# Kernel optimization log

Hardware: AMD Instinct MI355X
Metric: run time of the kernel (lower is better)

The kernel has to match this reference:

```python
import jax, jax.numpy as jnp
import numpy as np

B, L, H = 32, 1024, 512
NEG_INF = -1e30

def setup_inputs() -> dict:
    key = jax.random.key(0)
    k1, k2, k3, k4, k5 = jax.random.split(key, 5)
    c = jax.random.normal(k1, (B, L, H), dtype=jnp.float32)
    c_mask = jax.random.randint(k2, (B, L), 0, 2, dtype=jnp.int32)
    # xavier_uniform-like init scale for [H,1]: sqrt(6/(H+1))
    lim = float(np.sqrt(6.0 / (H + 1)))
    c_weight = jax.random.uniform(k3, (H, 1), minval=-lim, maxval=lim, dtype=jnp.float32)
    q_weight = jax.random.uniform(k4, (H, 1), minval=-lim, maxval=lim, dtype=jnp.float32)
    cq_weight = jax.random.uniform(k5, (1, 1, H), minval=-lim, maxval=lim, dtype=jnp.float32)
    bias = jnp.zeros((1,), dtype=jnp.float32)
    return {"c": c, "c_mask": c_mask, "c_weight": c_weight, "q_weight": q_weight,
            "cq_weight": cq_weight, "bias": bias}

def reference(c, c_mask, c_weight, q_weight, cq_weight, bias):
    m = c_mask.astype(jnp.float32)                     # [B,L]
    # similarity matrix (BiDAF trilinear decomposition), q == c here
    s0 = c @ c_weight                                  # [B,L,1]
    s1 = jnp.swapaxes(c @ q_weight, 1, 2)              # [B,1,L]
    s2 = jnp.einsum('blh,bmh->blm', c * cq_weight, c)  # [B,L,L]
    s = s0 + s1 + s2 + bias                            # [B,L,L]
    mask_row = m[:, None, :]                           # mask over dim=2 (keys)
    mask_col = m[:, :, None]                           # mask over dim=1
    s1p = jax.nn.softmax(mask_row * s + (1.0 - mask_row) * NEG_INF, axis=2)
    s2p = jax.nn.softmax(mask_col * s + (1.0 - mask_col) * NEG_INF, axis=1)
    a = s1p @ c                                        # [B,L,H]
    b = (s1p @ jnp.swapaxes(s2p, 1, 2)) @ c            # [B,L,H]
    return jnp.concatenate([c, a, c * a, c * b], axis=2)  # [B,L,4H]
```

## Files before the change

kernel.cpp:

```cpp
#include <hip/hip_runtime.h>
#include <hip/hip_bf16.h>
#include <stdint.h>

constexpr int Bb = 32;
constexpr int Ll = 1024;
constexpr int Hh = 512;

typedef __attribute__((ext_vector_type(8))) short short8;
typedef __attribute__((ext_vector_type(4))) short short4v;
typedef __attribute__((ext_vector_type(4))) float float4v;
typedef __attribute__((ext_vector_type(4))) int int4v;

__device__ inline short f2bf(float f) {
  union { float f; uint32_t u; } v; v.f = f;
  uint32_t r = (v.u + 0x7FFF + ((v.u >> 16) & 1)) >> 16;
  return (short)r;
}

#define MFMA(a, b, c) __builtin_amdgcn_mfma_f32_16x16x32_bf16(a, b, c, 0, 0, 0)

__device__ inline void gl_lds(const short* g, short* l) {
  __builtin_amdgcn_global_load_lds(
      (const __attribute__((address_space(1))) unsigned int*)g,
      (__attribute__((address_space(3))) unsigned int*)l, 16, 0, 0);
}

template <int ROWS>
__device__ inline void stage(short* lds, const short* g, int sk, int t) {
  const int w = t >> 6;
  const int kbg = (t & 7) ^ ((t >> 3) & 7);
#pragma unroll
  for (int r = 0; r < ROWS / 32; ++r) {
    int row = r * 32 + (t >> 3);
    gl_lds(g + (size_t)row * sk + kbg * 8, lds + (r * 32 + w * 8) * 64);
  }
}

__device__ inline short8 fld(const short* lds, int row, int kb) {
  return *(const short8*)(lds + row * 64 + ((kb ^ (row & 7)) << 3));
}

__global__ __launch_bounds__(256) void k_rowdots(
    const float* __restrict__ c, const float* __restrict__ cw,
    const float* __restrict__ qw, float* __restrict__ s0, float* __restrict__ s1) {
  int row = blockIdx.x * 4 + (threadIdx.x >> 6);
  int lane = threadIdx.x & 63;
  const float* cr = c + (size_t)row * Hh;
  float d0 = 0.f, d1 = 0.f;
#pragma unroll
  for (int i = 0; i < Hh / 64; ++i) {
    int h = lane + i * 64;
    float v = cr[h];
    d0 = fmaf(v, cw[h], d0);
    d1 = fmaf(v, qw[h], d1);
  }
#pragma unroll
  for (int off = 32; off > 0; off >>= 1) {
    d0 += __shfl_down(d0, off);
    d1 += __shfl_down(d1, off);
  }
  if (lane == 0) { s0[row] = d0; s1[row] = d1; }
}

__global__ __launch_bounds__(256) void k_cvt(
    const float* __restrict__ c, const float* __restrict__ cq,
    short* __restrict__ c16, short* __restrict__ cbq16) {
  size_t i8 = ((size_t)blockIdx.x * 256 + threadIdx.x) * 8;
  int h = (int)(i8 & (Hh - 1));
  float4v v0 = *(const float4v*)&c[i8];
  float4v v1 = *(const float4v*)&c[i8 + 4];
  float4v q0 = *(const float4v*)&cq[h];
  float4v q1 = *(const float4v*)&cq[h + 4];
  short8 a, bq;
#pragma unroll
  for (int j = 0; j < 4; ++j) {
    a[j] = f2bf(v0[j]);     a[4 + j] = f2bf(v1[j]);
    bq[j] = f2bf(v0[j] * q0[j]); bq[4 + j] = f2bf(v1[j] * q1[j]);
  }
  *(short8*)&c16[i8] = a;
  *(short8*)&cbq16[i8] = bq;
}

__global__ __launch_bounds__(256) void k_ct(const float* __restrict__ c,
                                            short* __restrict__ cT) {
  const int b = blockIdx.z, h0 = blockIdx.x * 64, l0 = blockIdx.y * 64;
  __shared__ short T[64 * 65];
  const int t = threadIdx.x, rl = t >> 4, c4 = (t & 15) * 4;
#pragma unroll
  for (int p = 0; p < 4; ++p) {
    int ll = rl + p * 16;
    float4v v = *(const float4v*)&c[((size_t)(b * Ll + l0 + ll)) * Hh + h0 + c4];
#pragma unroll
    for (int j = 0; j < 4; ++j) T[ll * 65 + c4 + j] = f2bf(v[j]);
  }
  __syncthreads();
#pragma unroll
  for (int p = 0; p < 4; ++p) {
    int hh = rl + p * 16;
    short4v o;
#pragma unroll
    for (int j = 0; j < 4; ++j) o[j] = T[(c4 + j) * 65 + hh];
    *(short4v*)&cT[((size_t)(b * Hh + h0 + hh)) * Ll + l0 + c4] = o;
  }
}

__global__ __launch_bounds__(256) void k_sgemm(
    const short* __restrict__ Aq, const short* __restrict__ Bc,
    const float* __restrict__ s0, const float* __restrict__ s1,
    const float* __restrict__ bias, const int* __restrict__ c_mask,
    float* __restrict__ S,
    float* __restrict__ rowpmax, float* __restrict__ rowpsum,
    float* __restrict__ colpmax, float* __restrict__ colpsum) {
  int flat = blockIdx.x + ((blockIdx.y + (blockIdx.z << 3)) << 3);
  flat = ((flat & 7) << 8) | (flat >> 3);
  const int b = flat >> 6, l0 = ((flat >> 3) & 7) << 7, m0 = (flat & 7) << 7;
  __shared__ __align__(16) short As[128 * 64];
  __shared__ __align__(16) short Bs[128 * 64];
  const int t = threadIdx.x, li = t & 63, w = t >> 6;
  const int wy = w >> 1, wx = w & 1, rr = li & 15, q = li >> 4;
  const short* Ag = Aq + ((size_t)b * Ll + l0) * Hh;
  const short* Bg = Bc + ((size_t)b * Ll + m0) * Hh;
  float4v acc[4][4];
#pragma unroll
  for (int i = 0; i < 4; ++i)
#pragma unroll
    for (int j = 0; j < 4; ++j) acc[i][j] = (float4v){0.f, 0.f, 0.f, 0.f};
  for (int kk = 0; kk < Hh; kk += 64) {
    stage<128>(As, Ag + kk, Hh, t);
    stage<128>(Bs, Bg + kk, Hh, t);
    __syncthreads();
#pragma unroll
    for (int ks = 0; ks < 2; ++ks) {
      int kb = ks * 4 + q;
      short8 af[4], bf4[4];
#pragma unroll
      for (int mt = 0; mt < 4; ++mt) af[mt] = fld(As, wy * 64 + mt * 16 + rr, kb);
#pragma unroll
      for (int nt = 0; nt < 4; ++nt) bf4[nt] = fld(Bs, wx * 64 + nt * 16 + rr, kb);
#pragma unroll
      for (int mt = 0; mt < 4; ++mt)
#pragma unroll
        for (int nt = 0; nt < 4; ++nt)
          acc[mt][nt] = MFMA(af[mt], bf4[nt], acc[mt][nt]);
    }
    __syncthreads();
  }
  const float bsc = bias[0];
  float s1v[4]; int mkm[4];
#pragma unroll
  for (int nt = 0; nt < 4; ++nt) {
    int m = m0 + wx * 64 + nt * 16 + rr;
    s1v[nt] = s1[b * Ll + m] + bsc;
    mkm[nt] = c_mask[b * Ll + m];
  }
  int mkl[4][4];
#pragma unroll
  for (int mt = 0; mt < 4; ++mt)
#pragma unroll
    for (int i = 0; i < 4; ++i) {
      int l = l0 + wy * 64 + mt * 16 + q * 4 + i;
      float s0v = s0[b * Ll + l];
      mkl[mt][i] = c_mask[b * Ll + l];
#pragma unroll
      for (int nt = 0; nt < 4; ++nt) acc[mt][nt][i] += s0v + s1v[nt];
    }
  float* Sb = S + (size_t)b * Ll * Ll;
#pragma unroll
  for (int nt = 0; nt < 4; ++nt) {
    int m = m0 + wx * 64 + nt * 16 + rr;
#pragma unroll
    for (int mt = 0; mt < 4; ++mt)
#pragma unroll
      for (int i = 0; i < 4; ++i) {
        int l = l0 + wy * 64 + mt * 16 + q * 4 + i;
        Sb[(size_t)l * Ll + m] = acc[mt][nt][i];
      }
  }
  float* red = (float*)As;
  const size_t rbase = (size_t)(m0 >> 7) * (Bb * Ll) + (size_t)b * Ll + l0;
  const size_t cbase = (size_t)(l0 >> 7) * (Bb * Ll) + (size_t)b * Ll + m0;
  float rv[16];
#pragma unroll
  for (int mt = 0; mt < 4; ++mt)
#pragma unroll
    for (int i = 0; i < 4; ++i) {
      float v = -INFINITY;
#pragma unroll
      for (int nt = 0; nt < 4; ++nt) v = mkm[nt] ? fmaxf(v, acc[mt][nt][i]) : v;
      rv[mt * 4 + i] = v;
    }
#pragma unroll
  for (int off = 1; off < 16; off <<= 1)
#pragma unroll
    for (int j = 0; j < 16; ++j) rv[j] = fmaxf(rv[j], __shfl_xor(rv[j], off));
  if (rr == 0)
#pragma unroll
    for (int j = 0; j < 16; ++j)
      red[wx * 128 + wy * 64 + (j >> 2) * 16 + q * 4 + (j & 3)] = rv[j];
  __syncthreads();
  if (t < 128) {
    float M = fmaxf(red[t], red[128 + t]);
    red[t] = M;
    rowpmax[rbase + t] = M;
  }
  __syncthreads();
#pragma unroll
  for (int mt = 0; mt < 4; ++mt)
#pragma unroll
    for (int i = 0; i < 4; ++i) {
      float M = red[wy * 64 + mt * 16 + q * 4 + i];
      float sacc = 0.f;
      if (M > -INFINITY) {
#pragma unroll
        for (int nt = 0; nt < 4; ++nt)
          sacc += mkm[nt] ? __expf(acc[mt][nt][i] - M) : 0.f;
      }
      rv[mt * 4 + i] = sacc;
    }
#pragma unroll
  for (int off = 1; off < 16; off <<= 1)
#pragma unroll
    for (int j = 0; j < 16; ++j) rv[j] += __shfl_xor(rv[j], off);
  __syncthreads();
  if (rr == 0)
#pragma unroll
    for (int j = 0; j < 16; ++j)
      red[wx * 128 + wy * 64 + (j >> 2) * 16 + q * 4 + (j & 3)] = rv[j];
  __syncthreads();
  if (t < 128) rowpsum[rbase + t] = red[t] + red[128 + t];
  float cv[4];
#pragma unroll
  for (int nt = 0; nt < 4; ++nt) {
    float v = -INFINITY;
#pragma unroll
    for (int mt = 0; mt < 4; ++mt)
#pragma unroll
      for (int i = 0; i < 4; ++i) v = mkl[mt][i] ? fmaxf(v, acc[mt][nt][i]) : v;
    cv[nt] = v;
  }
#pragma unroll
  for (int nt = 0; nt < 4; ++nt) {
    cv[nt] = fmaxf(cv[nt], __shfl_xor(cv[nt], 16));
    cv[nt] = fmaxf(cv[nt], __shfl_xor(cv[nt], 32));
  }
  __syncthreads();
  if (q == 0)
#pragma unroll
    for (int nt = 0; nt < 4; ++nt) red[wy * 128 + wx * 64 + nt * 16 + rr] = cv[nt];
  __syncthreads();
  if (t < 128) {
    float M = fmaxf(red[t], red[128 + t]);
    red[t] = M;
    colpmax[cbase + t] = M;
  }
  __syncthreads();
#pragma unroll
  for (int nt = 0; nt < 4; ++nt) {
    float M = red[wx * 64 + nt * 16 + rr];
    float sacc = 0.f;
    if (M > -INFINITY) {
#pragma unroll
      for (int mt = 0; mt < 4; ++mt)
#pragma unroll
        for (int i = 0; i < 4; ++i)
          sacc += mkl[mt][i] ? __expf(acc[mt][nt][i] - M) : 0.f;
    }
    cv[nt] = sacc;
  }
#pragma unroll
  for (int nt = 0; nt < 4; ++nt) {
    cv[nt] += __shfl_xor(cv[nt], 16);
    cv[nt] += __shfl_xor(cv[nt], 32);
  }
  __syncthreads();
  if (q == 0)
#pragma unroll
    for (int nt = 0; nt < 4; ++nt) red[wy * 128 + wx * 64 + nt * 16 + rr] = cv[nt];
  __syncthreads();
  if (t < 128) colpsum[cbase + t] = red[t] + red[128 + t];
}

__global__ __launch_bounds__(256) void k_comb(
    const float* __restrict__ pmax, const float* __restrict__ psum,
    float* __restrict__ omax, float* __restrict__ orcp) {
  int i = blockIdx.x * 256 + threadIdx.x;
  float M = -INFINITY;
#pragma unroll
  for (int k = 0; k < 8; ++k) M = fmaxf(M, pmax[k * (Bb * Ll) + i]);
  float s = 0.f;
#pragma unroll
  for (int k = 0; k < 8; ++k) {
    float pm = pmax[k * (Bb * Ll) + i];
    if (pm > -INFINITY) s += psum[k * (Bb * Ll) + i] * __expf(pm - M);
  }
  omax[i] = M;
  orcp[i] = 1.f / s;
}

__global__ __launch_bounds__(256) void k_p12(
    const float* __restrict__ S, const int* __restrict__ c_mask,
    const float* __restrict__ rowmax, const float* __restrict__ rowrcp,
    const float* __restrict__ colmax, const float* __restrict__ colrcp,
    short* __restrict__ P1, short* __restrict__ P2T) {
  const int b = blockIdx.z, m0 = blockIdx.x * 64, l0 = blockIdx.y * 64;
  __shared__ short T[64 * 65];
  const int t = threadIdx.x, rl = t >> 4, c4 = (t & 15) * 4;
  const float* Sb = S + (size_t)b * Ll * Ll;
  float4v cm = *(const float4v*)&colmax[b * Ll + m0 + c4];
  float4v cr = *(const float4v*)&colrcp[b * Ll + m0 + c4];
  int4v mkm = *(const int4v*)&c_mask[b * Ll + m0 + c4];
#pragma unroll
  for (int p = 0; p < 4; ++p) {
    int ll = rl + p * 16;
    int gl = b * Ll + l0 + ll;
    int mkl = c_mask[gl];
    float rm = rowmax[gl], rrc = rowrcp[gl];
    float4v v = *(const float4v*)&Sb[(size_t)(l0 + ll) * Ll + m0 + c4];
    short4v o1;
#pragma unroll
    for (int j = 0; j < 4; ++j) {
      o1[j] = mkm[j] ? f2bf(__expf(v[j] - rm) * rrc) : (short)0;
      T[ll * 65 + c4 + j] = mkl ? f2bf(__expf(v[j] - cm[j]) * cr[j]) : (short)0;
    }
    *(short4v*)&P1[(size_t)gl * Ll + m0 + c4] = o1;
  }
  __syncthreads();
#pragma unroll
  for (int p = 0; p < 4; ++p) {
    int mm = rl + p * 16;
    short4v o;
#pragma unroll
    for (int j = 0; j < 4; ++j) o[j] = T[(c4 + j) * 65 + mm];
    *(short4v*)&P2T[((size_t)(b * Ll + m0 + mm)) * Ll + l0 + c4] = o;
  }
}

__global__ __launch_bounds__(256) void k_ugemm(
    const short* __restrict__ P2T, const short* __restrict__ cT,
    short* __restrict__ uT) {
  int flat = blockIdx.x + ((blockIdx.y + (blockIdx.z << 3)) << 2);
  flat = ((flat & 7) << 7) | (flat >> 3);
  const int b = flat >> 5, m0 = ((flat >> 2) & 7) << 7, h0 = (flat & 3) << 7;
  __shared__ __align__(16) short As[128 * 64];
  __shared__ __align__(16) short Bs[128 * 64];
  const int t = threadIdx.x, li = t & 63, w = t >> 6;
  const int wy = w >> 1, wx = w & 1, rr = li & 15, q = li >> 4;
  const short* Ag = P2T + ((size_t)b * Ll + m0) * Ll;
  const short* Bg = cT + ((size_t)b * Hh + h0) * Ll;
  float4v acc[4][4];
#pragma unroll
  for (int i = 0; i < 4; ++i)
#pragma unroll
    for (int j = 0; j < 4; ++j) acc[i][j] = (float4v){0.f, 0.f, 0.f, 0.f};
  for (int kk = 0; kk < Ll; kk += 64) {
    stage<128>(As, Ag + kk, Ll, t);
    stage<128>(Bs, Bg + kk, Ll, t);
    __syncthreads();
#pragma unroll
    for (int ks = 0; ks < 2; ++ks) {
      int kb = ks * 4 + q;
      short8 af[4], bf4[4];
#pragma unroll
      for (int mt = 0; mt < 4; ++mt) af[mt] = fld(As, wy * 64 + mt * 16 + rr, kb);
#pragma unroll
      for (int nt = 0; nt < 4; ++nt) bf4[nt] = fld(Bs, wx * 64 + nt * 16 + rr, kb);
#pragma unroll
      for (int mt = 0; mt < 4; ++mt)
#pragma unroll
        for (int nt = 0; nt < 4; ++nt)
          acc[mt][nt] = MFMA(af[mt], bf4[nt], acc[mt][nt]);
    }
    __syncthreads();
  }
#pragma unroll
  for (int nt = 0; nt < 4; ++nt) {
    int h = h0 + wx * 64 + nt * 16 + rr;
#pragma unroll
    for (int mt = 0; mt < 4; ++mt) {
      int mb = m0 + wy * 64 + mt * 16 + q * 4;
      short4v o;
#pragma unroll
      for (int i = 0; i < 4; ++i) o[i] = f2bf(acc[mt][nt][i]);
      *(short4v*)&uT[((size_t)b * Hh + h) * Ll + mb] = o;
    }
  }
}

__global__ __launch_bounds__(256, 4) void k_abgemm(
    const short* __restrict__ P1, const short* __restrict__ cT,
    const short* __restrict__ uT, const float* __restrict__ c,
    float* __restrict__ out) {
  int flat = blockIdx.x + ((blockIdx.y + (blockIdx.z << 3)) << 3);
  flat = ((flat & 7) << 8) | (flat >> 3);
  const int b = flat >> 6, l0 = ((flat >> 3) & 7) << 7, h0 = (flat & 7) << 6;
  __shared__ __align__(16) short As[128 * 64];
  __shared__ __align__(16) short B1s[64 * 64];
  __shared__ __align__(16) short B2s[64 * 64];
  const int t = threadIdx.x, li = t & 63, w = t >> 6;
  const int wy = w >> 1, wx = w & 1, rr = li & 15, q = li >> 4;
  const short* Ag = P1 + ((size_t)b * Ll + l0) * Ll;
  const short* B1g = cT + ((size_t)b * Hh + h0) * Ll;
  const short* B2g = uT + ((size_t)b * Hh + h0) * Ll;
  float4v aa[4][2], ab[4][2];
#pragma unroll
  for (int i = 0; i < 4; ++i)
#pragma unroll
    for (int j = 0; j < 2; ++j) {
      aa[i][j] = (float4v){0.f, 0.f, 0.f, 0.f};
      ab[i][j] = (float4v){0.f, 0.f, 0.f, 0.f};
    }
  for (int kk = 0; kk < Ll; kk += 64) {
    stage<128>(As, Ag + kk, Ll, t);
    stage<64>(B1s, B1g + kk, Ll, t);
    stage<64>(B2s, B2g + kk, Ll, t);
    __syncthreads();
#pragma unroll
    for (int ks = 0; ks < 2; ++ks) {
      int kb = ks * 4 + q;
      short8 af[4], b1[2], b2[2];
#pragma unroll
      for (int mt = 0; mt < 4; ++mt) af[mt] = fld(As, wy * 64 + mt * 16 + rr, kb);
#pragma unroll
      for (int nt = 0; nt < 2; ++nt) {
        b1[nt] = fld(B1s, wx * 32 + nt * 16 + rr, kb);
        b2[nt] = fld(B2s, wx * 32 + nt * 16 + rr, kb);
      }
#pragma unroll
      for (int mt = 0; mt < 4; ++mt)
#pragma unroll
        for (int nt = 0; nt < 2; ++nt) {
          aa[mt][nt] = MFMA(af[mt], b1[nt], aa[mt][nt]);
          ab[mt][nt] = MFMA(af[mt], b2[nt], ab[mt][nt]);
        }
    }
    __syncthreads();
  }
#pragma unroll
  for (int nt = 0; nt < 2; ++nt) {
    int h = h0 + wx * 32 + nt * 16 + rr;
#pragma unroll
    for (int mt = 0; mt < 4; ++mt) {
#pragma unroll
      for (int i = 0; i < 4; ++i) {
        int l = l0 + wy * 64 + mt * 16 + q * 4 + i;
        float cv = c[((size_t)b * Ll + l) * Hh + h];
        size_t ob = ((size_t)b * Ll + l) * (size_t)(4 * Hh);
        float av = aa[mt][nt][i], bv = ab[mt][nt][i];
        out[ob + h] = cv;
        out[ob + Hh + h] = av;
        out[ob + 2 * Hh + h] = cv * av;
        out[ob + 3 * Hh + h] = cv * bv;
      }
    }
  }
}

extern "C" void kernel_launch(void* const* d_in, const int* in_sizes, int n_in,
                              void* d_out, int out_size, void* d_ws, size_t ws_size,
                              hipStream_t stream) {
  const float* c = (const float*)d_in[0];
  const int* c_mask = (const int*)d_in[1];
  const float* c_weight = (const float*)d_in[2];
  const float* q_weight = (const float*)d_in[3];
  const float* cq = (const float*)d_in[4];
  const float* bias = (const float*)d_in[5];
  float* out = (float*)d_out;

  char* ws = (char*)d_ws;
  float* S = (float*)ws;
  short* uT = (short*)ws;
  short* cT16 = (short*)(ws + 134217728ull);
  short* c16 = (short*)(ws + 167772160ull);
  short* P1 = (short*)(ws + 167772160ull);
  short* cbq16 = (short*)(ws + 201326592ull);
  short* P2T = (short*)(ws + 234881024ull);
  float* rowpmax = (float*)(ws + 234881024ull);
  float* rowpsum = (float*)(ws + 234881024ull + 1048576ull);
  float* colpmax = (float*)(ws + 234881024ull + 2097152ull);
  float* colpsum = (float*)(ws + 234881024ull + 3145728ull);
  float* st = (float*)(ws + 301989888ull);
  float* s0 = st;
  float* s1 = st + 32768;
  float* rowmax = st + 65536;
  float* rowrcp = st + 98304;
  float* colmax = st + 131072;
  float* colrcp = st + 163840;

  k_rowdots<<<dim3(Bb * Ll / 4), dim3(256), 0, stream>>>(c, c_weight, q_weight, s0, s1);
  k_cvt<<<dim3(8192), dim3(256), 0, stream>>>(c, cq, c16, cbq16);
  k_ct<<<dim3(Hh / 64, Ll / 64, Bb), dim3(256), 0, stream>>>(c, cT16);
  k_sgemm<<<dim3(Ll / 128, Ll / 128, Bb), dim3(256), 0, stream>>>(
      cbq16, c16, s0, s1, bias, c_mask, S, rowpmax, rowpsum, colpmax, colpsum);
  k_comb<<<dim3(Bb * Ll / 256), dim3(256), 0, stream>>>(rowpmax, rowpsum, rowmax, rowrcp);
  k_comb<<<dim3(Bb * Ll / 256), dim3(256), 0, stream>>>(colpmax, colpsum, colmax, colrcp);
  k_p12<<<dim3(Ll / 64, Ll / 64, Bb), dim3(256), 0, stream>>>(
      S, c_mask, rowmax, rowrcp, colmax, colrcp, P1, P2T);
  k_ugemm<<<dim3(Hh / 128, Ll / 128, Bb), dim3(256), 0, stream>>>(P2T, cT16, uT);
  k_abgemm<<<dim3(Hh / 64, Ll / 128, Bb), dim3(256), 0, stream>>>(P1, cT16, uT, c, out);
}
```

Measured before the change: 688.9 us.

## Double-buffer LDS in GEMM kernels, fuse conversion kernels, merge combine launches

Adds two-stage LDS double buffering to the score, u and a/b GEMMs, so global-to-LDS staging of the next K tile is issued before computing the current one and load latency overlaps MFMA work. Folds the bf16 conversion of c and c*cq into the transpose kernel, which removes one full pass over the fp32 input. Merges the row and column softmax combine kernels into one launch and drops the min-blocks hint on the a/b GEMM. The cost is double the LDS per block (64KB), which can lower occupancy.

After: 719.4 us. 4.4% more time.

```diff
diff --git a/kernel.cpp b/kernel.cpp
--- a/kernel.cpp
+++ b/kernel.cpp
@@ -62,36 +62,28 @@
   if (lane == 0) { s0[row] = d0; s1[row] = d1; }
 }
 
-__global__ __launch_bounds__(256) void k_cvt(
+__global__ __launch_bounds__(256) void k_ct(
     const float* __restrict__ c, const float* __restrict__ cq,
-    short* __restrict__ c16, short* __restrict__ cbq16) {
-  size_t i8 = ((size_t)blockIdx.x * 256 + threadIdx.x) * 8;
-  int h = (int)(i8 & (Hh - 1));
-  float4v v0 = *(const float4v*)&c[i8];
-  float4v v1 = *(const float4v*)&c[i8 + 4];
-  float4v q0 = *(const float4v*)&cq[h];
-  float4v q1 = *(const float4v*)&cq[h + 4];
-  short8 a, bq;
-#pragma unroll
-  for (int j = 0; j < 4; ++j) {
-    a[j] = f2bf(v0[j]);     a[4 + j] = f2bf(v1[j]);
-    bq[j] = f2bf(v0[j] * q0[j]); bq[4 + j] = f2bf(v1[j] * q1[j]);
-  }
-  *(short8*)&c16[i8] = a;
-  *(short8*)&cbq16[i8] = bq;
-}
-
-__global__ __launch_bounds__(256) void k_ct(const float* __restrict__ c,
-                                            short* __restrict__ cT) {
+    short* __restrict__ cT, short* __restrict__ c16, short* __restrict__ cbq16) {
   const int b = blockIdx.z, h0 = blockIdx.x * 64, l0 = blockIdx.y * 64;
   __shared__ short T[64 * 65];
   const int t = threadIdx.x, rl = t >> 4, c4 = (t & 15) * 4;
+  float4v qv = *(const float4v*)&cq[h0 + c4];
 #pragma unroll
   for (int p = 0; p < 4; ++p) {
     int ll = rl + p * 16;
-    float4v v = *(const float4v*)&c[((size_t)(b * Ll + l0 + ll)) * Hh + h0 + c4];
-#pragma unroll
-    for (int j = 0; j < 4; ++j) T[ll * 65 + c4 + j] = f2bf(v[j]);
+    size_t gi = ((size_t)(b * Ll + l0 + ll)) * Hh + h0 + c4;
+    float4v v = *(const float4v*)&c[gi];
+    short4v o, oq;
+#pragma unroll
+    for (int j = 0; j < 4; ++j) {
+      short bv = f2bf(v[j]);
+      T[ll * 65 + c4 + j] = bv;
+      o[j] = bv;
+      oq[j] = f2bf(v[j] * qv[j]);
+    }
+    *(short4v*)&c16[gi] = o;
+    *(short4v*)&cbq16[gi] = oq;
   }
   __syncthreads();
 #pragma unroll
@@ -114,8 +106,8 @@
   int flat = blockIdx.x + ((blockIdx.y + (blockIdx.z << 3)) << 3);
   flat = ((flat & 7) << 8) | (flat >> 3);
   const int b = flat >> 6, l0 = ((flat >> 3) & 7) << 7, m0 = (flat & 7) << 7;
-  __shared__ __align__(16) short As[128 * 64];
-  __shared__ __align__(16) short Bs[128 * 64];
+  __shared__ __align__(16) short As[2][128 * 64];
+  __shared__ __align__(16) short Bs[2][128 * 64];
   const int t = threadIdx.x, li = t & 63, w = t >> 6;
   const int wy = w >> 1, wx = w & 1, rr = li & 15, q = li >> 4;
   const short* Ag = Aq + ((size_t)b * Ll + l0) * Hh;
@@ -125,18 +117,24 @@
   for (int i = 0; i < 4; ++i)
 #pragma unroll
     for (int j = 0; j < 4; ++j) acc[i][j] = (float4v){0.f, 0.f, 0.f, 0.f};
-  for (int kk = 0; kk < Hh; kk += 64) {
-    stage<128>(As, Ag + kk, Hh, t);
-    stage<128>(Bs, Bg + kk, Hh, t);
-    __syncthreads();
+  stage<128>(As[0], Ag, Hh, t);
+  stage<128>(Bs[0], Bg, Hh, t);
+  __syncthreads();
+  for (int it = 0; it < Hh / 64; ++it) {
+    if (it + 1 < Hh / 64) {
+      stage<128>(As[(it + 1) & 1], Ag + (it + 1) * 64, Hh, t);
+      stage<128>(Bs[(it + 1) & 1], Bg + (it + 1) * 64, Hh, t);
+    }
+    const short* Ab = As[it & 1];
+    const short* Bbuf = Bs[it & 1];
 #pragma unroll
     for (int ks = 0; ks < 2; ++ks) {
       int kb = ks * 4 + q;
       short8 af[4], bf4[4];
 #pragma unroll
-      for (int mt = 0; mt < 4; ++mt) af[mt] = fld(As, wy * 64 + mt * 16 + rr, kb);
-#pragma unroll
-      for (int nt = 0; nt < 4; ++nt) bf4[nt] = fld(Bs, wx * 64 + nt * 16 + rr, kb);
+      for (int mt = 0; mt < 4; ++mt) af[mt] = fld(Ab, wy * 64 + mt * 16 + rr, kb);
+#pragma unroll
+      for (int nt = 0; nt < 4; ++nt) bf4[nt] = fld(Bbuf, wx * 64 + nt * 16 + rr, kb);
 #pragma unroll
       for (int mt = 0; mt < 4; ++mt)
 #pragma unroll
@@ -280,10 +278,16 @@
   if (t < 128) colpsum[cbase + t] = red[t] + red[128 + t];
 }
 
-__global__ __launch_bounds__(256) void k_comb(
-    const float* __restrict__ pmax, const float* __restrict__ psum,
-    float* __restrict__ omax, float* __restrict__ orcp) {
+__global__ __launch_bounds__(256) void k_comb2(
+    const float* __restrict__ rpm, const float* __restrict__ rps,
+    const float* __restrict__ cpm, const float* __restrict__ cps,
+    float* __restrict__ rmax, float* __restrict__ rrcp,
+    float* __restrict__ cmax, float* __restrict__ crcp) {
   int i = blockIdx.x * 256 + threadIdx.x;
+  const float* pmax = blockIdx.y ? cpm : rpm;
+  const float* psum = blockIdx.y ? cps : rps;
+  float* omax = blockIdx.y ? cmax : rmax;
+  float* orcp = blockIdx.y ? crcp : rrcp;
   float M = -INFINITY;
 #pragma unroll
   for (int k = 0; k < 8; ++k) M = fmaxf(M, pmax[k * (Bb * Ll) + i]);
@@ -341,8 +345,8 @@
   int flat = blockIdx.x + ((blockIdx.y + (blockIdx.z << 3)) << 2);
   flat = ((flat & 7) << 7) | (flat >> 3);
   const int b = flat >> 5, m0 = ((flat >> 2) & 7) << 7, h0 = (flat & 3) << 7;
-  __shared__ __align__(16) short As[128 * 64];
-  __shared__ __align__(16) short Bs[128 * 64];
+  __shared__ __align__(16) short As[2][128 * 64];
+  __shared__ __align__(16) short Bs[2][128 * 64];
   const int t = threadIdx.x, li = t & 63, w = t >> 6;
   const int wy = w >> 1, wx = w & 1, rr = li & 15, q = li >> 4;
   const short* Ag = P2T + ((size_t)b * Ll + m0) * Ll;
@@ -352,18 +356,24 @@
   for (int i = 0; i < 4; ++i)
 #pragma unroll
     for (int j = 0; j < 4; ++j) acc[i][j] = (float4v){0.f, 0.f, 0.f, 0.f};
-  for (int kk = 0; kk < Ll; kk += 64) {
-    stage<128>(As, Ag + kk, Ll, t);
-    stage<128>(Bs, Bg + kk, Ll, t);
-    __syncthreads();
+  stage<128>(As[0], Ag, Ll, t);
+  stage<128>(Bs[0], Bg, Ll, t);
+  __syncthreads();
+  for (int it = 0; it < Ll / 64; ++it) {
+    if (it + 1 < Ll / 64) {
+      stage<128>(As[(it + 1) & 1], Ag + (it + 1) * 64, Ll, t);
+      stage<128>(Bs[(it + 1) & 1], Bg + (it + 1) * 64, Ll, t);
+    }
+    const short* Ab = As[it & 1];
+    const short* Bbuf = Bs[it & 1];
 #pragma unroll
     for (int ks = 0; ks < 2; ++ks) {
       int kb = ks * 4 + q;
       short8 af[4], bf4[4];
 #pragma unroll
-      for (int mt = 0; mt < 4; ++mt) af[mt] = fld(As, wy * 64 + mt * 16 + rr, kb);
-#pragma unroll
-      for (int nt = 0; nt < 4; ++nt) bf4[nt] = fld(Bs, wx * 64 + nt * 16 + rr, kb);
+      for (int mt = 0; mt < 4; ++mt) af[mt] = fld(Ab, wy * 64 + mt * 16 + rr, kb);
+#pragma unroll
+      for (int nt = 0; nt < 4; ++nt) bf4[nt] = fld(Bbuf, wx * 64 + nt * 16 + rr, kb);
 #pragma unroll
       for (int mt = 0; mt < 4; ++mt)
 #pragma unroll
@@ -386,16 +396,16 @@
   }
 }
 
-__global__ __launch_bounds__(256, 4) void k_abgemm(
+__global__ __launch_bounds__(256) void k_abgemm(
     const short* __restrict__ P1, const short* __restrict__ cT,
     const short* __restrict__ uT, const float* __restrict__ c,
     float* __restrict__ out) {
   int flat = blockIdx.x + ((blockIdx.y + (blockIdx.z << 3)) << 3);
   flat = ((flat & 7) << 8) | (flat >> 3);
   const int b = flat >> 6, l0 = ((flat >> 3) & 7) << 7, h0 = (flat & 7) << 6;
-  __shared__ __align__(16) short As[128 * 64];
-  __shared__ __align__(16) short B1s[64 * 64];
-  __shared__ __align__(16) short B2s[64 * 64];
+  __shared__ __align__(16) short As[2][128 * 64];
+  __shared__ __align__(16) short B1s[2][64 * 64];
+  __shared__ __align__(16) short B2s[2][64 * 64];
   const int t = threadIdx.x, li = t & 63, w = t >> 6;
   const int wy = w >> 1, wx = w & 1, rr = li & 15, q = li >> 4;
   const short* Ag = P1 + ((size_t)b * Ll + l0) * Ll;
@@ -409,21 +419,29 @@
       aa[i][j] = (float4v){0.f, 0.f, 0.f, 0.f};
       ab[i][j] = (float4v){0.f, 0.f, 0.f, 0.f};
     }
-  for (int kk = 0; kk < Ll; kk += 64) {
-    stage<128>(As, Ag + kk, Ll, t);
-    stage<64>(B1s, B1g + kk, Ll, t);
-    stage<64>(B2s, B2g + kk, Ll, t);
-    __syncthreads();
+  stage<128>(As[0], Ag, Ll, t);
+  stage<64>(B1s[0], B1g, Ll, t);
+  stage<64>(B2s[0], B2g, Ll, t);
+  __syncthreads();
+  for (int it = 0; it < Ll / 64; ++it) {
+    if (it + 1 < Ll / 64) {
+      stage<128>(As[(it + 1) & 1], Ag + (it + 1) * 64, Ll, t);
+      stage<64>(B1s[(it + 1) & 1], B1g + (it + 1) * 64, Ll, t);
+      stage<64>(B2s[(it + 1) & 1], B2g + (it + 1) * 64, Ll, t);
+    }
+    const short* Ab = As[it & 1];
+    const short* B1b = B1s[it & 1];
+    const short* B2b = B2s[it & 1];
 #pragma unroll
     for (int ks = 0; ks < 2; ++ks) {
       int kb = ks * 4 + q;
       short8 af[4], b1[2], b2[2];
 #pragma unroll
-      for (int mt = 0; mt < 4; ++mt) af[mt] = fld(As, wy * 64 + mt * 16 + rr, kb);
+      for (int mt = 0; mt < 4; ++mt) af[mt] = fld(Ab, wy * 64 + mt * 16 + rr, kb);
 #pragma unroll
       for (int nt = 0; nt < 2; ++nt) {
-        b1[nt] = fld(B1s, wx * 32 + nt * 16 + rr, kb);
-        b2[nt] = fld(B2s, wx * 32 + nt * 16 + rr, kb);
+        b1[nt] = fld(B1b, wx * 32 + nt * 16 + rr, kb);
+        b2[nt] = fld(B2b, wx * 32 + nt * 16 + rr, kb);
       }
 #pragma unroll
       for (int mt = 0; mt < 4; ++mt)
@@ -487,12 +505,11 @@
   float* colrcp = st + 163840;
 
   k_rowdots<<<dim3(Bb * Ll / 4), dim3(256), 0, stream>>>(c, c_weight, q_weight, s0, s1);
-  k_cvt<<<dim3(8192), dim3(256), 0, stream>>>(c, cq, c16, cbq16);
-  k_ct<<<dim3(Hh / 64, Ll / 64, Bb), dim3(256), 0, stream>>>(c, cT16);
+  k_ct<<<dim3(Hh / 64, Ll / 64, Bb), dim3(256), 0, stream>>>(c, cq, cT16, c16, cbq16);
   k_sgemm<<<dim3(Ll / 128, Ll / 128, Bb), dim3(256), 0, stream>>>(
       cbq16, c16, s0, s1, bias, c_mask, S, rowpmax, rowpsum, colpmax, colpsum);
-  k_comb<<<dim3(Bb * Ll / 256), dim3(256), 0, stream>>>(rowpmax, rowpsum, rowmax, rowrcp);
-  k_comb<<<dim3(Bb * Ll / 256), dim3(256), 0, stream>>>(colpmax, colpsum, colmax, colrcp);
+  k_comb2<<<dim3(Bb * Ll / 256, 2), dim3(256), 0, stream>>>(
+      rowpmax, rowpsum, colpmax, colpsum, rowmax, rowrcp, colmax, colrcp);
   k_p12<<<dim3(Ll / 64, Ll / 64, Bb), dim3(256), 0, stream>>>(
       S, c_mask, rowmax, rowrcp, colmax, colrcp, P1, P2T);
   k_ugemm<<<dim3(Hh / 128, Ll / 128, Bb), dim3(256), 0, stream>>>(P2T, cT16, uT);
```
